# Performance work log

Measured on AMD Instinct MI355X. Metric: run time of the kernel, lower is better.

Reference implementation:

```python
import jax, jax.numpy as jnp
import numpy as np

N_E, E_DIM = 8192, 256
N = 32768

def setup_inputs() -> dict:
    key = jax.random.key(0)
    kz, kw = jax.random.split(key)
    z = jax.random.normal(kz, (N, E_DIM), dtype=jnp.float32)
    # nn.Embedding weight initialized uniform(-1/n_e, 1/n_e)
    W = jax.random.uniform(kw, (N_E, E_DIM), dtype=jnp.float32,
                           minval=-1.0 / N_E, maxval=1.0 / N_E)
    return {"z": z, "W": W}

def reference(z, W):
    # z: [N, D] (already flat since rank-2), W: [K, D]
    z_flat = z.reshape(z.shape[0], -1)
    # squared euclidean distance via ||z||^2 + ||w||^2 - 2 z.w
    d = (jnp.sum(z_flat ** 2, axis=1, keepdims=True)
         + jnp.sum(W ** 2, axis=1)
         - 2.0 * jnp.einsum('nd,kd->nk', z_flat, W))  # [N, K]
    idx = jnp.argmin(d, axis=1)                        # [N]
    z_q = W[idx].reshape(z.shape)                      # gather codebook vectors
    # straight-through estimator
    z_q = z + jax.lax.stop_gradient(z_q - z)
    loss = jnp.zeros((z.shape[0],), dtype=z.dtype)
    return z_q, idx, loss
```

## Files before the change

### kernel.cpp

```cpp
#include <hip/hip_runtime.h>
#include <stdint.h>


constexpr int N = 32768;
constexpr int K = 8192;
constexpr int D = 256;
constexpr int CAP = 12;
constexpr int SCAP = 20;
constexpr int TCAP = CAP + SCAP;
constexpr int NT = 36;
#define MARGIN 1.0e-4f

typedef __attribute__((ext_vector_type(8))) short short8v;
typedef __attribute__((ext_vector_type(4))) float float4v;

__device__ inline short f2bf(float f) {
    unsigned u = __float_as_uint(f);
    unsigned r = (u + 0x7FFFu + ((u >> 16) & 1u)) >> 16;
    return (short)r;
}
__device__ inline unsigned encf(float x) {
    unsigned u = __float_as_uint(x);
    return (u & 0x80000000u) ? ~u : (u | 0x80000000u);
}
__device__ inline float decf(unsigned e) {
    unsigned u = (e & 0x80000000u) ? (e & 0x7FFFFFFFu) : ~e;
    return __uint_as_float(u);
}
__device__ inline void load_lds16(const void* g, void* l) {
    __builtin_amdgcn_global_load_lds(
        (const __attribute__((address_space(1))) void*)g,
        (__attribute__((address_space(3))) void*)l, 16, 0, 0);
}

__global__ __launch_bounds__(256) void fuse_pack(const float* __restrict__ X,
                                                 short* __restrict__ Xf,
                                                 float* __restrict__ s_out,
                                                 unsigned long long* __restrict__ best,
                                                 unsigned char* __restrict__ flags) {
    __shared__ float raw[64][260];
    __shared__ float hres[64][2];
    const int t = threadIdx.x;
    const size_t base = (size_t)blockIdx.x * 64 * D;
#pragma unroll
    for (int it = 0; it < 16; ++it) {
        int idx = it * 256 + t;
        int r = idx >> 6, c = idx & 63;
        float4 v = ((const float4*)(X + base))[idx];
        *(float4*)&raw[r][c * 4] = v;
    }
    __syncthreads();
    if (t < 128) {
        const int row = t >> 1, h = t & 1;
        const float* ph = raw[row] + h * 128;
        float r8[8];
#pragma unroll
        for (int j = 0; j < 8; ++j) r8[j] = __fmul_rn(ph[j], ph[j]);
        for (int i = 8; i < 128; i += 8)
#pragma unroll
            for (int j = 0; j < 8; ++j)
                r8[j] = __fadd_rn(r8[j], __fmul_rn(ph[i + j], ph[i + j]));
        hres[row][h] = __fadd_rn(__fadd_rn(__fadd_rn(r8[0], r8[1]), __fadd_rn(r8[2], r8[3])),
                                 __fadd_rn(__fadd_rn(r8[4], r8[5]), __fadd_rn(r8[6], r8[7])));
    }
    {
        const int lane = t & 63, w = t >> 6, l4 = lane >> 4, l15 = lane & 15;
        const int row = w * 16 + l15;
#pragma unroll
        for (int s = 0; s < 8; ++s) {
            const float* src = &raw[row][s * 32 + l4 * 8];
            float4 v0 = *(const float4*)src;
            float4 v1 = *(const float4*)(src + 4);
            short8v o;
            o[0] = f2bf(v0.x); o[1] = f2bf(v0.y); o[2] = f2bf(v0.z); o[3] = f2bf(v0.w);
            o[4] = f2bf(v1.x); o[5] = f2bf(v1.y); o[6] = f2bf(v1.z); o[7] = f2bf(v1.w);
            *(short8v*)(Xf + ((size_t)(blockIdx.x * 4 + w) * 8 + s) * 512 + lane * 8) = o;
        }
    }
    __syncthreads();
    if (t < 64) {
        s_out[blockIdx.x * 64 + t] = __fadd_rn(hres[t][0], hres[t][1]);
        if (best) {
            best[blockIdx.x * 64 + t] = 0xFFFFFFFFFFFFFFFFull;
            flags[blockIdx.x * 64 + t] = 0;
        }
    }
}

__global__ __launch_bounds__(256, 2) void vq_screen(
    const short* __restrict__ Zf, const short* __restrict__ Wf,
    const float* __restrict__ s_w, const float* __restrict__ s_z,
    const float* __restrict__ Z, const float* __restrict__ W,
    unsigned* __restrict__ spill,
    unsigned long long* __restrict__ best, unsigned char* __restrict__ gflags)
{
    __shared__ short Bs[2][4][8][512];
    __shared__ unsigned rowmax[256];
    __shared__ unsigned ccnt[256];
    __shared__ unsigned candkm[256][CAP];

    const int t = threadIdx.x, w = t >> 6, lane = t & 63;
    const int l4 = lane >> 4, l15 = lane & 15;
    const int q = blockIdx.x & 3, rg = blockIdx.x >> 2;
    const int n0 = rg * 256;
    const int kq0 = q * 2048;
    unsigned* const spillB = spill + (size_t)blockIdx.x * 256 * SCAP;

    rowmax[t] = encf(-1e30f);
    ccnt[t] = 0u;

    short8v af[4][8];
    {
        const int R = (n0 >> 4) + w * 4;
#pragma unroll
        for (int g = 0; g < 4; ++g)
#pragma unroll
            for (int s = 0; s < 8; ++s)
                af[g][s] = *(const short8v*)(Zf + ((size_t)(R + g) * 8 + s) * 512 + lane * 8);
    }

    float maxv[16];
#pragma unroll
    for (int i = 0; i < 16; ++i) maxv[i] = -1e30f;

    {
        const int col16 = (kq0 >> 4) + w;
        const short* gB = Wf + (size_t)col16 * 8 * 512 + lane * 8;
#pragma unroll
        for (int s = 0; s < 8; ++s)
            load_lds16(gB + s * 512, &Bs[0][w][s][0]);
    }

    for (int tt = 0; tt < NT; ++tt) {
        const int cur = tt & 1;
        __syncthreads();
        if (tt + 1 < NT) {
            const int ktn = (tt + 1 < 4) ? (tt + 1) : (tt + 1 - 4);
            const int col16 = (kq0 >> 4) + ktn * 4 + w;
            const short* gB = Wf + (size_t)col16 * 8 * 512 + lane * 8;
#pragma unroll
            for (int s = 0; s < 8; ++s)
                load_lds16(gB + s * 512, &Bs[cur ^ 1][w][s][0]);
        }

        float4v acc[4][4];
#pragma unroll
        for (int i = 0; i < 4; ++i)
#pragma unroll
            for (int j = 0; j < 4; ++j)
#pragma unroll
                for (int r = 0; r < 4; ++r) acc[i][j][r] = 0.f;

#pragma unroll
        for (int s = 0; s < 8; ++s) {
            short8v bf[4];
#pragma unroll
            for (int j = 0; j < 4; ++j)
                bf[j] = *(const short8v*)&Bs[cur][j][s][lane * 8];
#pragma unroll
            for (int i = 0; i < 4; ++i)
#pragma unroll
                for (int j = 0; j < 4; ++j)
                    acc[i][j] = __builtin_amdgcn_mfma_f32_16x16x32_bf16(af[i][s], bf[j], acc[i][j], 0, 0, 0);
        }

        if (tt < 4) {
#pragma unroll
            for (int i = 0; i < 4; ++i)
#pragma unroll
                for (int r = 0; r < 4; ++r) {
                    const int slot = i * 4 + r;
                    float mj = fmaxf(fmaxf(acc[i][0][r], acc[i][1][r]),
                                     fmaxf(acc[i][2][r], acc[i][3][r]));
                    if (mj > maxv[slot]) {
                        maxv[slot] = mj;
                        atomicMax(&rowmax[w * 64 + i * 16 + l4 * 4 + r], encf(mj));
                    }
                }
            continue;
        }

        const int kt = tt - 4;
#pragma unroll
        for (int i = 0; i < 4; ++i) {
            uint4 rm = *(const uint4*)&rowmax[w * 64 + i * 16 + l4 * 4];
            maxv[i * 4 + 0] = fmaxf(maxv[i * 4 + 0], decf(rm.x));
            maxv[i * 4 + 1] = fmaxf(maxv[i * 4 + 1], decf(rm.y));
            maxv[i * 4 + 2] = fmaxf(maxv[i * 4 + 2], decf(rm.z));
            maxv[i * 4 + 3] = fmaxf(maxv[i * 4 + 3], decf(rm.w));
        }
        const int kb = kq0 + kt * 64 + l15;
#pragma unroll
        for (int i = 0; i < 4; ++i) {
#pragma unroll
            for (int r = 0; r < 4; ++r) {
                const int slot = i * 4 + r;
                const int rowL = w * 64 + i * 16 + l4 * 4 + r;
                float v0 = acc[i][0][r], v1 = acc[i][1][r];
                float v2 = acc[i][2][r], v3 = acc[i][3][r];
                float mj = fmaxf(fmaxf(v0, v1), fmaxf(v2, v3));
                if (mj > maxv[slot]) {
                    maxv[slot] = mj;
                    atomicMax(&rowmax[rowL], encf(mj));
                }
                float th = maxv[slot] - MARGIN;
                if (mj >= th) {
                    float vv[4] = {v0, v1, v2, v3};
#pragma unroll
                    for (int j = 0; j < 4; ++j) {
                        if (vv[j] >= th) {
                            unsigned c = atomicAdd(&ccnt[rowL], 1u);
                            unsigned pk = (encf(vv[j]) & 0xFFFF0000u) | (unsigned)(kb + 16 * j);
                            if (c < CAP) candkm[rowL][c] = pk;
                            else if (c < TCAP) spillB[rowL * SCAP + (c - CAP)] = pk;
                        }
                    }
                }
            }
        }
    }

    __threadfence_block();
    __syncthreads();
    {
        const int n = n0 + t;
        unsigned cnt = ccnt[t];
        if (cnt > (unsigned)TCAP) {
            gflags[n] = 1;
        } else if (cnt > 0) {
            const float thr = decf(rowmax[t]) - MARGIN;
            const float sz = s_z[n];
            const float4* zr = (const float4*)(Z + (size_t)n * D);
            float bd = 1e30f; int bk = 0x7FFFFFFF;
            for (unsigned c = 0; c < cnt; ++c) {
                const unsigned cm = (c < CAP) ? candkm[t][c] : spillB[t * SCAP + (c - CAP)];
                if (decf((cm & 0xFFFF0000u) + 0x10000u) < thr) continue;
                const int k = (int)(cm & 0x1FFFu);
                const float4* wr = (const float4*)(W + (size_t)k * D);
                float ax = 0.f, ay = 0.f, az = 0.f, aw = 0.f;
                for (int qq = 0; qq < 64; ++qq) {
                    float4 zv = zr[qq], wv = wr[qq];
                    ax = fmaf(zv.x, wv.x, ax);
                    ay = fmaf(zv.y, wv.y, ay);
                    az = fmaf(zv.z, wv.z, az);
                    aw = fmaf(zv.w, wv.w, aw);
                }
                float dot = (ax + ay) + (az + aw);
                float dd = (sz + s_w[k]) - 2.0f * dot;
                if (dd < bd || (dd == bd && k < bk)) { bd = dd; bk = k; }
            }
            atomicMin(&best[n], ((unsigned long long)encf(bd) << 32) | (unsigned)bk);
        }
    }
}

__global__ __launch_bounds__(256) void vq_fallback(
    const float* __restrict__ Z, const float* __restrict__ W,
    const float* __restrict__ s_z, const float* __restrict__ s_w,
    const unsigned char* __restrict__ flags, unsigned long long* __restrict__ best)
{
    __shared__ int anyf;
    const int t = threadIdx.x;
    const int rbase = blockIdx.x * 64;
    if (t == 0) anyf = 0;
    __syncthreads();
    if (t < 64 && flags[rbase + t]) anyf = 1;
    __syncthreads();
    if (!anyf) return;
    for (int r = 0; r < 64; ++r) {
        if (!flags[rbase + r]) continue;
        const int n = rbase + r;
        const float sz = s_z[n];
        const float4* zr = (const float4*)(Z + (size_t)n * D);
        float bd = 1e30f; int bk = 0x7FFFFFFF;
        for (int k = t; k < K; k += 256) {
            const float4* wr = (const float4*)(W + (size_t)k * D);
            float ax = 0.f, ay = 0.f, az = 0.f, aw = 0.f;
            for (int qq = 0; qq < 64; ++qq) {
                float4 zv = zr[qq], wv = wr[qq];
                ax = fmaf(zv.x, wv.x, ax);
                ay = fmaf(zv.y, wv.y, ay);
                az = fmaf(zv.z, wv.z, az);
                aw = fmaf(zv.w, wv.w, aw);
            }
            float dd = (sz + s_w[k]) - 2.0f * ((ax + ay) + (az + aw));
            if (dd < bd || (dd == bd && k < bk)) { bd = dd; bk = k; }
        }
        atomicMin(&best[n], ((unsigned long long)encf(bd) << 32) | (unsigned)bk);
    }
}

__global__ __launch_bounds__(256) void out_kernel(const float* __restrict__ W,
                                                  const unsigned long long* __restrict__ best,
                                                  float* __restrict__ zq,
                                                  float* __restrict__ idx_f,
                                                  float* __restrict__ loss) {
    const int w = threadIdx.x >> 6, lane = threadIdx.x & 63;
#pragma unroll
    for (int i = 0; i < 4; ++i) {
        const int r = blockIdx.x * 16 + w * 4 + i;
        const int k = (int)(unsigned)(best[r] & 0xFFFFFFFFull);
        float4 v = ((const float4*)(W + (size_t)k * D))[lane];
        ((float4*)(zq + (size_t)r * D))[lane] = v;
        if (lane == 0) {
            idx_f[r] = (float)k;
            loss[r] = 0.f;
        }
    }
}

extern "C" void kernel_launch(void* const* d_in, const int* in_sizes, int n_in,
                              void* d_out, int out_size, void* d_ws, size_t ws_size,
                              hipStream_t stream) {
    const float* Z = (const float*)d_in[0];
    const float* W = (const float*)d_in[1];

    float* zq    = (float*)d_out;
    float* idx_f = zq + (size_t)N * D;
    float* loss  = idx_f + N;

    short* Zf = (short*)d_out;
    short* Wf = (short*)((char*)d_out + (size_t)16 * 1024 * 1024);
    unsigned* spill = (unsigned*)((char*)d_out + (size_t)20 * 1024 * 1024);

    float* s_w = (float*)d_ws;
    float* s_z = s_w + K;
    unsigned long long* best = (unsigned long long*)(s_z + N);
    unsigned char* flags = (unsigned char*)(best + N);

    fuse_pack<<<N / 64, 256, 0, stream>>>(Z, Zf, s_z, best, flags);
    fuse_pack<<<K / 64, 256, 0, stream>>>(W, Wf, s_w, nullptr, nullptr);
    vq_screen<<<512, 256, 0, stream>>>(Zf, Wf, s_w, s_z, Z, W, spill, best, flags);
    vq_fallback<<<N / 64, 256, 0, stream>>>(Z, W, s_z, s_w, flags, best);
    out_kernel<<<N / 16, 256, 0, stream>>>(W, best, zq, idx_f, loss);
}
```

Baseline: 377.0 us.

## Restructure screen kernel: Z tile in LDS, codebook streamed to registers per wave

Each block now handles 64 rows and half the codebook. The Z tile is kept in LDS and each wave streams its own 1024-column codebook slice from global memory straight into registers with a software double buffer, instead of staging codebook tiles in double-buffered LDS behind block-wide barriers. The grid doubles, occupancy is raised to 3 blocks per CU, and the exact rescoring of candidates is split across 4 threads per row. The goal is to remove per-tile syncthreads and improve latency hiding, at the cost of more global traffic to re-read W per wave and fewer shared max updates, which could admit more candidates.

```diff
diff --git a/kernel.cpp b/kernel.cpp
--- a/kernel.cpp
+++ b/kernel.cpp
@@ -5,10 +5,9 @@
 constexpr int N = 32768;
 constexpr int K = 8192;
 constexpr int D = 256;
-constexpr int CAP = 12;
-constexpr int SCAP = 20;
+constexpr int CAP = 16;
+constexpr int SCAP = 16;
 constexpr int TCAP = CAP + SCAP;
-constexpr int NT = 36;
 #define MARGIN 1.0e-4f
 
 typedef __attribute__((ext_vector_type(8))) short short8v;
@@ -87,61 +86,48 @@
     }
 }
 
-__global__ __launch_bounds__(256, 2) void vq_screen(
+__global__ __launch_bounds__(256, 3) void vq_screen(
     const short* __restrict__ Zf, const short* __restrict__ Wf,
     const float* __restrict__ s_w, const float* __restrict__ s_z,
     const float* __restrict__ Z, const float* __restrict__ W,
     unsigned* __restrict__ spill,
     unsigned long long* __restrict__ best, unsigned char* __restrict__ gflags)
 {
-    __shared__ short Bs[2][4][8][512];
-    __shared__ unsigned rowmax[256];
-    __shared__ unsigned ccnt[256];
-    __shared__ unsigned candkm[256][CAP];
+    __shared__ short As[4][8][512];
+    __shared__ unsigned rowmax[64];
+    __shared__ unsigned ccnt[64];
+    __shared__ unsigned candkm[64][CAP];
 
     const int t = threadIdx.x, w = t >> 6, lane = t & 63;
     const int l4 = lane >> 4, l15 = lane & 15;
-    const int q = blockIdx.x & 3, rg = blockIdx.x >> 2;
-    const int n0 = rg * 256;
-    const int kq0 = q * 2048;
-    unsigned* const spillB = spill + (size_t)blockIdx.x * 256 * SCAP;
-
-    rowmax[t] = encf(-1e30f);
-    ccnt[t] = 0u;
-
-    short8v af[4][8];
+    const int rg = blockIdx.x >> 1;
+    const int hh = blockIdx.x & 1;
+    const int n0 = rg * 64;
+    const int kw0 = hh * 4096 + w * 1024;
+    unsigned* const spillB = spill + (size_t)blockIdx.x * 64 * SCAP;
+
+    if (t < 64) { rowmax[t] = encf(-1e30f); ccnt[t] = 0u; }
     {
-        const int R = (n0 >> 4) + w * 4;
-#pragma unroll
-        for (int g = 0; g < 4; ++g)
-#pragma unroll
-            for (int s = 0; s < 8; ++s)
-                af[g][s] = *(const short8v*)(Zf + ((size_t)(R + g) * 8 + s) * 512 + lane * 8);
-    }
+        const short* gA = Zf + ((size_t)(rg * 4 + w) * 8) * 512 + lane * 8;
+#pragma unroll
+        for (int s = 0; s < 8; ++s)
+            load_lds16(gA + s * 512, &As[w][s][0]);
+    }
+    __syncthreads();
 
     float maxv[16];
 #pragma unroll
     for (int i = 0; i < 16; ++i) maxv[i] = -1e30f;
 
-    {
-        const int col16 = (kq0 >> 4) + w;
-        const short* gB = Wf + (size_t)col16 * 8 * 512 + lane * 8;
-#pragma unroll
-        for (int s = 0; s < 8; ++s)
-            load_lds16(gB + s * 512, &Bs[0][w][s][0]);
-    }
-
-    for (int tt = 0; tt < NT; ++tt) {
-        const int cur = tt & 1;
-        __syncthreads();
-        if (tt + 1 < NT) {
-            const int ktn = (tt + 1 < 4) ? (tt + 1) : (tt + 1 - 4);
-            const int col16 = (kq0 >> 4) + ktn * 4 + w;
-            const short* gB = Wf + (size_t)col16 * 8 * 512 + lane * 8;
-#pragma unroll
-            for (int s = 0; s < 8; ++s)
-                load_lds16(gB + s * 512, &Bs[cur ^ 1][w][s][0]);
-        }
+    for (int tt = 0; tt < 17; ++tt) {
+        const int ttc = (tt == 0) ? 0 : (tt - 1);
+        const int c16base = (kw0 >> 4) + ttc * 4;
+        const short* bbase = Wf + lane * 8;
+
+        short8v bfA[4], bfB[4];
+#pragma unroll
+        for (int j = 0; j < 4; ++j)
+            bfA[j] = *(const short8v*)(bbase + ((size_t)(c16base + j) * 8 + 0) * 512);
 
         float4v acc[4][4];
 #pragma unroll
@@ -153,18 +139,25 @@
 
 #pragma unroll
         for (int s = 0; s < 8; ++s) {
-            short8v bf[4];
-#pragma unroll
-            for (int j = 0; j < 4; ++j)
-                bf[j] = *(const short8v*)&Bs[cur][j][s][lane * 8];
+            const short8v* cur = (s & 1) ? bfB : bfA;
+            short8v* nxt = (s & 1) ? bfA : bfB;
+            if (s < 7) {
+#pragma unroll
+                for (int j = 0; j < 4; ++j)
+                    nxt[j] = *(const short8v*)(bbase + ((size_t)(c16base + j) * 8 + s + 1) * 512);
+            }
+            short8v af[4];
 #pragma unroll
             for (int i = 0; i < 4; ++i)
+                af[i] = *(const short8v*)&As[i][s][lane * 8];
+#pragma unroll
+            for (int i = 0; i < 4; ++i)
 #pragma unroll
                 for (int j = 0; j < 4; ++j)
-                    acc[i][j] = __builtin_amdgcn_mfma_f32_16x16x32_bf16(af[i][s], bf[j], acc[i][j], 0, 0, 0);
-        }
-
-        if (tt < 4) {
+                    acc[i][j] = __builtin_amdgcn_mfma_f32_16x16x32_bf16(af[i], cur[j], acc[i][j], 0, 0, 0);
+        }
+
+        if (tt == 0) {
 #pragma unroll
             for (int i = 0; i < 4; ++i)
 #pragma unroll
@@ -174,28 +167,27 @@
                                      fmaxf(acc[i][2][r], acc[i][3][r]));
                     if (mj > maxv[slot]) {
                         maxv[slot] = mj;
-                        atomicMax(&rowmax[w * 64 + i * 16 + l4 * 4 + r], encf(mj));
+                        atomicMax(&rowmax[i * 16 + l4 * 4 + r], encf(mj));
                     }
                 }
             continue;
         }
 
-        const int kt = tt - 4;
 #pragma unroll
         for (int i = 0; i < 4; ++i) {
-            uint4 rm = *(const uint4*)&rowmax[w * 64 + i * 16 + l4 * 4];
+            uint4 rm = *(const uint4*)&rowmax[i * 16 + l4 * 4];
             maxv[i * 4 + 0] = fmaxf(maxv[i * 4 + 0], decf(rm.x));
             maxv[i * 4 + 1] = fmaxf(maxv[i * 4 + 1], decf(rm.y));
             maxv[i * 4 + 2] = fmaxf(maxv[i * 4 + 2], decf(rm.z));
             maxv[i * 4 + 3] = fmaxf(maxv[i * 4 + 3], decf(rm.w));
         }
-        const int kb = kq0 + kt * 64 + l15;
+        const int kb = kw0 + ttc * 64 + l15;
 #pragma unroll
         for (int i = 0; i < 4; ++i) {
 #pragma unroll
             for (int r = 0; r < 4; ++r) {
                 const int slot = i * 4 + r;
-                const int rowL = w * 64 + i * 16 + l4 * 4 + r;
+                const int rowL = i * 16 + l4 * 4 + r;
                 float v0 = acc[i][0][r], v1 = acc[i][1][r];
                 float v2 = acc[i][2][r], v3 = acc[i][3][r];
                 float mj = fmaxf(fmaxf(v0, v1), fmaxf(v2, v3));
@@ -223,17 +215,18 @@
     __threadfence_block();
     __syncthreads();
     {
-        const int n = n0 + t;
-        unsigned cnt = ccnt[t];
+        const int row = t & 63, part = t >> 6;
+        const int n = n0 + row;
+        unsigned cnt = ccnt[row];
         if (cnt > (unsigned)TCAP) {
-            gflags[n] = 1;
+            if (part == 0) gflags[n] = 1;
         } else if (cnt > 0) {
-            const float thr = decf(rowmax[t]) - MARGIN;
+            const float thr = decf(rowmax[row]) - MARGIN;
             const float sz = s_z[n];
             const float4* zr = (const float4*)(Z + (size_t)n * D);
             float bd = 1e30f; int bk = 0x7FFFFFFF;
-            for (unsigned c = 0; c < cnt; ++c) {
-                const unsigned cm = (c < CAP) ? candkm[t][c] : spillB[t * SCAP + (c - CAP)];
+            for (unsigned c = part; c < cnt; c += 4) {
+                const unsigned cm = (c < CAP) ? candkm[row][c] : spillB[row * SCAP + (c - CAP)];
                 if (decf((cm & 0xFFFF0000u) + 0x10000u) < thr) continue;
                 const int k = (int)(cm & 0x1FFFu);
                 const float4* wr = (const float4*)(W + (size_t)k * D);
@@ -249,7 +242,8 @@
                 float dd = (sz + s_w[k]) - 2.0f * dot;
                 if (dd < bd || (dd == bd && k < bk)) { bd = dd; bk = k; }
             }
-            atomicMin(&best[n], ((unsigned long long)encf(bd) << 32) | (unsigned)bk);
+            if (bk != 0x7FFFFFFF)
+                atomicMin(&best[n], ((unsigned long long)encf(bd) << 32) | (unsigned)bk);
         }
     }
 }
@@ -330,7 +324,7 @@
 
     fuse_pack<<<N / 64, 256, 0, stream>>>(Z, Zf, s_z, best, flags);
     fuse_pack<<<K / 64, 256, 0, stream>>>(W, Wf, s_w, nullptr, nullptr);
-    vq_screen<<<512, 256, 0, stream>>>(Zf, Wf, s_w, s_z, Z, W, spill, best, flags);
+    vq_screen<<<1024, 256, 0, stream>>>(Zf, Wf, s_w, s_z, Z, W, spill, best, flags);
     vq_fallback<<<N / 64, 256, 0, stream>>>(Z, W, s_z, s_w, flags, best);
     out_kernel<<<N / 16, 256, 0, stream>>>(W, best, zq, idx_f, loss);
 }
```

New measurement: 349.4 us. 1.08x faster.
